# Kernel optimization log

Measured on AMD Instinct MI355X. Metric: run time of the kernel, lower is better.

Reference implementation:

```python
import jax, jax.numpy as jnp
import numpy as np

B, T, K = 512, 1024, 48


def setup_inputs() -> dict:
    key = jax.random.key(0)
    k1, k2, k3, k4, k5, k6 = jax.random.split(key, 6)
    return {
        "emission_scores": jax.random.normal(k1, (B, T, K), dtype=jnp.float32),
        "lengths": jax.random.randint(k2, (B,), 1, T + 1, dtype=jnp.int64),
        "tags": jax.random.randint(k3, (B, T), 0, K, dtype=jnp.int64),
        "prior": 0.1 * jax.random.normal(k4, (K,), dtype=jnp.float32),
        "transition": 0.1 * jax.random.normal(k5, (K, K), dtype=jnp.float32),
        "final_transition": 0.1 * jax.random.normal(k6, (K,), dtype=jnp.float32),
    }


def _partition_function(emission_scores, lengths, prior, transition, final_transition):
    batch, timesteps, num_tags = emission_scores.shape
    # alpha_0[b, i] = emis[b, 0, i] + prior[i]
    alpha0 = emission_scores[:, 0, :] + prior[None, :]

    def step(prev_alpha, emis_t):
        # alpha_t[b, i] = logsumexp_j(prev_alpha[b, j] + transition[i, j]) + emis_t[b, i]
        a = jax.nn.logsumexp(prev_alpha[:, None, :] + transition[None, :, :], axis=2)
        a = a + emis_t
        return a, a

    emis_rest = jnp.swapaxes(emission_scores, 0, 1)[1:]  # [T-1, B, K]
    _, alphas = jax.lax.scan(step, alpha0, emis_rest)
    alphas = jnp.concatenate([alpha0[None], alphas], axis=0)  # [T, B, K]
    alpha_final = alphas[lengths - 1, jnp.arange(batch)]  # [B, K] at last valid step
    alpha_final = alpha_final + final_transition[None, :]
    return jax.nn.logsumexp(alpha_final, axis=1)


def _score_path(emission_scores, lengths, tags, prior, transition, final_transition):
    batch, timesteps, num_tags = emission_scores.shape
    emis_tag = jnp.take_along_axis(emission_scores, tags[:, :, None], axis=2)[..., 0]  # [B, T]
    trans = transition[tags[:, 1:], tags[:, :-1]]  # [B, T-1]
    pr = prior[tags[:, 0]][:, None]  # [B, 1]
    scores = jnp.concatenate([pr, trans], axis=1) + emis_tag  # [B, T]
    valid = jnp.arange(timesteps)[None, :] < lengths[:, None]  # True for t < length
    scores = jnp.where(valid, scores, 0.0)
    final_tags = tags[jnp.arange(batch), lengths - 1]
    return jnp.sum(scores, axis=1) + final_transition[final_tags]


def reference(emission_scores, lengths, tags, prior, transition, final_transition):
    lengths = jnp.clip(lengths, 1, None)
    logZ = _partition_function(emission_scores, lengths, prior, transition, final_transition)
    path = _score_path(emission_scores, lengths, tags, prior, transition, final_transition)
    return jnp.mean(logZ - path)
```

## Files before the change

kernel.cpp:

```cpp
#include <hip/hip_runtime.h>


#define BB    512
#define TT    1024
#define KK    48
#define GG    16
#define NGRP  32
#define NSLOT 16
#define SLOTB (13 * GG * 16)
#define PHASE 8
#define BLKT  256

typedef __attribute__((ext_vector_type(4))) short bf16x4;
typedef __attribute__((ext_vector_type(4))) float f32x4;
typedef __attribute__((ext_vector_type(4))) int   i32x4;

__device__ __forceinline__ f32x4 mfma16(bf16x4 a, bf16x4 b, f32x4 c) {
#if __has_builtin(__builtin_amdgcn_mfma_f32_16x16x16bf16_1k)
    return __builtin_amdgcn_mfma_f32_16x16x16bf16_1k(a, b, c, 0, 0, 0);
#else
    f32x4 d;
    asm volatile("v_mfma_f32_16x16x16_bf16 %0, %1, %2, %3"
                 : "=v"(d) : "v"(a), "v"(b), "v"(c));
    return d;
#endif
}

#if __has_builtin(__builtin_amdgcn_cvt_pk_bf16_f32)
typedef __attribute__((ext_vector_type(2))) __bf16 bf16x2_v;
__device__ __forceinline__ unsigned pk2(float lo, float hi) {
    union { bf16x2_v v; unsigned u; } x;
    x.v = __builtin_amdgcn_cvt_pk_bf16_f32(lo, hi);
    return x.u;
}
#else
__device__ __forceinline__ unsigned pk2(float lo, float hi) {
    return __builtin_amdgcn_perm(__float_as_uint(hi) + 0x8000u,
                                 __float_as_uint(lo) + 0x8000u,
                                 0x07060302u);
}
#endif
__device__ __forceinline__ bf16x4 pack4(float a, float b, float c, float d) {
    union { unsigned u[2]; bf16x4 v; } x;
    x.u[0] = pk2(a, b);
    x.u[1] = pk2(c, d);
    return x.v;
}

#if __has_builtin(__builtin_amdgcn_permlane16_swap)
__device__ __forceinline__ float swap16_max(float x) {
    auto p = __builtin_amdgcn_permlane16_swap(__float_as_int(x),
                                              __float_as_int(x), false, false);
    return fmaxf(__int_as_float(p[0]), __int_as_float(p[1]));
}
__device__ __forceinline__ float swap16_sum(float x) {
    auto p = __builtin_amdgcn_permlane16_swap(__float_as_int(x),
                                              __float_as_int(x), false, false);
    return __int_as_float(p[0]) + __int_as_float(p[1]);
}
#else
__device__ __forceinline__ float swap16_max(float x) { return fmaxf(x, __shfl_xor(x, 16, 64)); }
__device__ __forceinline__ float swap16_sum(float x) { return x + __shfl_xor(x, 16, 64); }
#endif
#if __has_builtin(__builtin_amdgcn_permlane32_swap)
__device__ __forceinline__ float swap32_max(float x) {
    auto p = __builtin_amdgcn_permlane32_swap(__float_as_int(x),
                                              __float_as_int(x), false, false);
    return fmaxf(__int_as_float(p[0]), __int_as_float(p[1]));
}
__device__ __forceinline__ float swap32_sum(float x) {
    auto p = __builtin_amdgcn_permlane32_swap(__float_as_int(x),
                                              __float_as_int(x), false, false);
    return __int_as_float(p[0]) + __int_as_float(p[1]);
}
#else
__device__ __forceinline__ float swap32_max(float x) { return fmaxf(x, __shfl_xor(x, 32, 64)); }
__device__ __forceinline__ float swap32_sum(float x) { return x + __shfl_xor(x, 32, 64); }
#endif

__device__ __forceinline__ float wave_reduce_sum(float v) {
    #pragma unroll
    for (int off = 32; off > 0; off >>= 1)
        v += __shfl_xor(v, off, 64);
    return v;
}

__global__ __launch_bounds__(BLKT, 1) void crf_main_kernel(
    const float* __restrict__ emis,
    const int*   __restrict__ lengths,
    const int*   __restrict__ tags,
    const float* __restrict__ prior,
    const float* __restrict__ trans,
    const float* __restrict__ finalT,
    float*       __restrict__ ws)
{
    __shared__ __align__(16) unsigned char ring[NSLOT * SLOTB];
    __shared__ __align__(16) int prodCnt4[4];
    __shared__ int consCnt;

    const int tid  = threadIdx.x;
    const int wv   = tid >> 6;
    const int lane = tid & 63;

    if (blockIdx.x >= NGRP) {
        const int b = blockIdx.x - NGRP;
        int len = lengths[b];
        len = (len < 1) ? 1 : (len > TT ? TT : len);
        const float* eb = emis + (size_t)b * TT * KK;
        const int*   tg = tags + (size_t)b * TT;
        float ps = 0.0f;
        for (int t = tid; t < len; t += BLKT) {
            int cur = tg[t];
            float ev = eb[(size_t)t * KK + cur];
            float tr = (t == 0) ? prior[cur] : trans[cur * KK + tg[t - 1]];
            ps += ev + tr;
        }
        ps = wave_reduce_sum(ps);
        float* red = (float*)ring;
        if (lane == 0) red[wv] = ps;
        __syncthreads();
        if (tid == 0)
            ws[BB + b] = red[0] + red[1] + red[2] + red[3] + finalT[tg[len - 1]];
        return;
    }

    const int g = blockIdx.x;
    __builtin_amdgcn_s_setprio(1);

    if (tid == 0) {
        prodCnt4[0] = 0; prodCnt4[1] = 0; prodCnt4[2] = 0; prodCnt4[3] = 0;
        consCnt = 0;
    }
    __syncthreads();

    int myLen = lengths[g * GG + (lane & 15)];
    myLen = (myLen < 1) ? 1 : (myLen > TT ? TT : myLen);
    int gmax = myLen;
    #pragma unroll
    for (int off = 32; off > 0; off >>= 1) {
        int o = __shfl_xor(gmax, off, 64);
        gmax = (o > gmax) ? o : gmax;
    }
    const int nsteps = gmax - 1;
    const int nphase = (nsteps + PHASE - 1) / PHASE;

    if (wv >= 1) {
        const float* gp[3]; int lo[3];
        #pragma unroll
        for (int j = 0; j < 3; ++j) {
            int lidx = lane + 64 * j;
            int s    = lidx / 12;
            int kg   = lidx - s * 12;
            gp[j]    = emis + (size_t)(g * GG + s) * (TT * KK) + kg * 4;
            lo[j]    = (s * 13 + kg) * 16;
        }
        const int sA = wv - 1;
        float4 LA[9], LB[9];

#define PLOADX(Lb, KP)                                                     \
        {                                                                  \
            _Pragma("unroll")                                              \
            for (int h = 0; h < 3; ++h) {                                  \
                int s = sA + 3 * h;                                        \
                if (s < PHASE) {                                           \
                    int t  = 1 + (KP) * PHASE + s;                         \
                    int tc = (t > nsteps) ? nsteps : t;                    \
                    _Pragma("unroll")                                      \
                    for (int j = 0; j < 3; ++j)                            \
                        Lb[h * 3 + j] = *reinterpret_cast<const float4*>(  \
                            gp[j] + (size_t)tc * KK);                      \
                }                                                          \
            }                                                              \
        }

#define PSTORE(Lb, SB)                                                     \
        {                                                                  \
            _Pragma("unroll")                                              \
            for (int h = 0; h < 3; ++h) {                                  \
                int s = sA + 3 * h;                                        \
                if (s < PHASE) {                                           \
                    unsigned char* bp =                                    \
                        &ring[(((SB) + s) & (NSLOT - 1)) * SLOTB];         \
                    _Pragma("unroll")                                      \
                    for (int j = 0; j < 3; ++j) {                          \
                        float4 l = Lb[h * 3 + j];                          \
                        float4 e;                                          \
                        e.x = __expf(l.x); e.y = __expf(l.y);              \
                        e.z = __expf(l.z); e.w = __expf(l.w);              \
                        *reinterpret_cast<float4*>(bp + lo[j]) = e;        \
                    }                                                      \
                }                                                          \
            }                                                              \
        }

        PLOADX(LA, 0);
        PLOADX(LB, 1);
        volatile int* vc = &consCnt;
        for (int k0 = 0; k0 < nphase; k0 += 2) {
            while (*vc < k0 - 1) __builtin_amdgcn_s_sleep(1);
            asm volatile("" ::: "memory");
            PSTORE(LA, 1);
            asm volatile("s_waitcnt lgkmcnt(0)" ::: "memory");
            if (lane == 0) *(volatile int*)&prodCnt4[sA] = k0 + 1;
            asm volatile("" ::: "memory");
            PLOADX(LA, k0 + 2);
            if (k0 + 1 < nphase) {
                while (*vc < k0) __builtin_amdgcn_s_sleep(1);
                asm volatile("" ::: "memory");
                PSTORE(LB, 9);
                asm volatile("s_waitcnt lgkmcnt(0)" ::: "memory");
                if (lane == 0) *(volatile int*)&prodCnt4[sA] = k0 + 2;
                asm volatile("" ::: "memory");
                PLOADX(LB, k0 + 3);
            }
        }
#undef PLOADX
#undef PSTORE
        return;
    }

    const int col   = lane & 15;
    const int grp   = lane >> 4;
    const int rbase = grp * 4;
    const int seq   = g * GG + col;
    const int lenn1 = myLen - 1;

    bf16x4 A[3][3];
    #pragma unroll
    for (int mt = 0; mt < 3; ++mt) {
        #pragma unroll
        for (int kt = 0; kt < 3; ++kt) {
            float4 tv = *reinterpret_cast<const float4*>(
                trans + (size_t)(mt * 16 + col) * KK + kt * 16 + rbase);
            A[mt][kt] = pack4(__expf(tv.x), __expf(tv.y),
                              __expf(tv.z), __expf(tv.w));
        }
    }

    f32x4 EF[3];
    #pragma unroll
    for (int mt = 0; mt < 3; ++mt) {
        float4 fv = *reinterpret_cast<const float4*>(finalT + mt * 16 + rbase);
        EF[mt][0] = __expf(fv.x); EF[mt][1] = __expf(fv.y);
        EF[mt][2] = __expf(fv.z); EF[mt][3] = __expf(fv.w);
    }

    const float* ebase = emis + (size_t)seq * TT * KK + rbase;

    float c;
    float zcap = 0.0f;
    bf16x4 Bt0, Bt1, Bt2;
    {
        f32x4 a0[3];
        #pragma unroll
        for (int mt = 0; mt < 3; ++mt) {
            f32x4 ev = *reinterpret_cast<const f32x4*>(ebase + mt * 16);
            f32x4 pv = *reinterpret_cast<const f32x4*>(prior + mt * 16 + rbase);
            a0[mt] = ev + pv;
        }
        float mx = fmaxf(
            fmaxf(fmaxf(fmaxf(a0[0][0], a0[0][1]), fmaxf(a0[0][2], a0[0][3])),
                  fmaxf(fmaxf(a0[1][0], a0[1][1]), fmaxf(a0[1][2], a0[1][3]))),
            fmaxf(fmaxf(a0[2][0], a0[2][1]), fmaxf(a0[2][2], a0[2][3])));
        mx = swap16_max(mx);
        mx = swap32_max(mx);
        c = mx;
        #pragma unroll
        for (int mt = 0; mt < 3; ++mt) {
            #pragma unroll
            for (int e = 0; e < 4; ++e) a0[mt][e] = __expf(a0[mt][e] - c);
        }
        if (__ballot(lenn1 == 0)) {
            f32x4 Sv = a0[0] * EF[0] + a0[1] * EF[1] + a0[2] * EF[2];
            float S = (Sv[0] + Sv[1]) + (Sv[2] + Sv[3]);
            S = swap16_sum(S);
            S = swap32_sum(S);
            if (lenn1 == 0) zcap = c + __logf(S);
        }
        Bt0 = pack4(a0[0][0], a0[0][1], a0[0][2], a0[0][3]);
        Bt1 = pack4(a0[1][0], a0[1][1], a0[1][2], a0[1][3]);
        Bt2 = pack4(a0[2][0], a0[2][1], a0[2][2], a0[2][3]);
    }

    const int foff = col * 52 + grp * 4;
    const f32x4 zero4 = {0.f, 0.f, 0.f, 0.f};

#define XLOAD(dst, SLOT)                                                   \
        {                                                                  \
            const float* sp = reinterpret_cast<const float*>(              \
                ring + (SLOT) * SLOTB) + foff;                             \
            dst[0] = *reinterpret_cast<const f32x4*>(sp);                  \
            dst[1] = *reinterpret_cast<const f32x4*>(sp + 16);             \
            dst[2] = *reinterpret_cast<const f32x4*>(sp + 32);             \
        }

#define CPHASE(K_, SB)                                                       \
    {                                                                        \
        const int kc = (K_);                                                 \
        for (;;) {                            \
            i32x4 f = *(volatile i32x4*)prodCnt4;                            \
            if (f[0] >= kc + 1 && f[1] >= kc + 1 && f[2] >= kc + 1) break;   \
        }                                                                    \
        asm volatile("" ::: "memory");                                       \
        const int t0 = 1 + kc * PHASE;                                       \
        f32x4 Xq[PHASE + 2][3];                                              \
        XLOAD(Xq[0], ((SB) + 0) & (NSLOT - 1));                              \
        XLOAD(Xq[1], ((SB) + 1) & (NSLOT - 1));                              \
        _Pragma("unroll")                                                    \
        for (int s8 = 0; s8 < PHASE; ++s8) {                                 \
            if (s8 + 2 < PHASE)                        \
                XLOAD(Xq[s8 + 2], ((SB) + s8 + 2) & (NSLOT - 1));            \
            if (s8 == PHASE - 1) {                                           \
                  \
                asm volatile("s_waitcnt lgkmcnt(0)" ::: "memory");           \
                if (lane == 0) *(volatile int*)&consCnt = kc + 1;            \
                asm volatile("" ::: "memory");                               \
            }                                                                \
            const int t = t0 + s8;                \
            f32x4 D0 = mfma16(A[0][0], Bt0, zero4);                          \
            f32x4 D1 = mfma16(A[1][0], Bt0, zero4);                          \
            f32x4 D2 = mfma16(A[2][0], Bt0, zero4);                          \
            D0 = mfma16(A[0][1], Bt1, D0);                                   \
            D1 = mfma16(A[1][1], Bt1, D1);                                   \
            D2 = mfma16(A[2][1], Bt1, D2);                                   \
            D0 = mfma16(A[0][2], Bt2, D0);                                   \
            D1 = mfma16(A[1][2], Bt2, D1);                                   \
            D2 = mfma16(A[2][2], Bt2, D2);                                   \
            f32x4 Wa = D0 * Xq[s8][0];              \
            f32x4 Wb = D1 * Xq[s8][1];                                       \
            f32x4 Wc = D2 * Xq[s8][2];                                       \
            if (s8 == PHASE - 1) {                    \
                float mx = fmaxf(                                            \
                    fmaxf(fmaxf(fmaxf(Wa[0], Wa[1]), fmaxf(Wa[2], Wa[3])),   \
                          fmaxf(fmaxf(Wb[0], Wb[1]), fmaxf(Wb[2], Wb[3]))),  \
                    fmaxf(fmaxf(Wc[0], Wc[1]), fmaxf(Wc[2], Wc[3])));        \
                mx = swap16_max(mx);                                         \
                mx = swap32_max(mx);                                         \
                c += __logf(mx);                                             \
                float rm = __builtin_amdgcn_rcpf(mx);                        \
                Wa *= rm; Wb *= rm; Wc *= rm;                                \
            }                                                                \
            if (__ballot(t == lenn1)) {                    \
                f32x4 Sv = Wa * EF[0] + Wb * EF[1] + Wc * EF[2];             \
                float S = (Sv[0] + Sv[1]) + (Sv[2] + Sv[3]);                 \
                S = swap16_sum(S);                                           \
                S = swap32_sum(S);                                           \
                if (t == lenn1) zcap = c + __logf(S);                        \
            }                                                                \
            Bt0 = pack4(Wa[0], Wa[1], Wa[2], Wa[3]);                         \
            Bt1 = pack4(Wb[0], Wb[1], Wb[2], Wb[3]);                         \
            Bt2 = pack4(Wc[0], Wc[1], Wc[2], Wc[3]);                         \
        }                                                                    \
    }

    for (int k0 = 0; k0 < nphase; k0 += 2) {
        CPHASE(k0, 1);
        if (k0 + 1 < nphase) CPHASE(k0 + 1, 9);
    }
#undef CPHASE
#undef XLOAD

    if (lane < GG) ws[seq] = zcap;
}

__global__ __launch_bounds__(512) void reduce_mean_kernel(
    const float* __restrict__ ws, float* __restrict__ out)
{
    __shared__ float sm[8];
    int tid = threadIdx.x;
    float x = ws[tid] - ws[BB + tid];
    x = wave_reduce_sum(x);
    if ((tid & 63) == 0) sm[tid >> 6] = x;
    __syncthreads();
    if (tid < 8) {
        float y = sm[tid];
        y += __shfl_xor(y, 1, 64);
        y += __shfl_xor(y, 2, 64);
        y += __shfl_xor(y, 4, 64);
        if (tid == 0) out[0] = y * (1.0f / 512.0f);
    }
}

extern "C" void kernel_launch(void* const* d_in, const int* in_sizes, int n_in,
                              void* d_out, int out_size, void* d_ws, size_t ws_size,
                              hipStream_t stream) {
    const float* emis    = (const float*)d_in[0];
    const int*   lengths = (const int*)  d_in[1];
    const int*   tags    = (const int*)  d_in[2];
    const float* prior   = (const float*)d_in[3];
    const float* trans   = (const float*)d_in[4];
    const float* finalT  = (const float*)d_in[5];

    float* ws  = (float*)d_ws;
    float* out = (float*)d_out;

    crf_main_kernel<<<NGRP + BB, BLKT, 0, stream>>>(emis, lengths, tags, prior,
                                                    trans, finalT, ws);
    reduce_mean_kernel<<<1, 512, 0, stream>>>(ws, out);
}
```

Before: 303.8 us.

## Process two sequence groups per consumer wave with interleaved MFMA chains

Each consumer block now handles 32 sequences as two independent 16-column recurrences, interleaving their MFMA chains so one chain's latency is hidden behind the other. The number of group blocks is halved, the phase shrinks from 8 to 4 steps, and the ring shrinks to 8 slots. Producer waves compute exp before waiting, and the consumer uses inline-asm LDS reads with explicit waitcnt and templated capture dispatch. The trade-off is fewer concurrent recurrence blocks and more register pressure per wave, in exchange for better MFMA pipeline utilisation.

```diff
diff --git a/kernel.cpp b/kernel.cpp
--- a/kernel.cpp
+++ b/kernel.cpp
@@ -4,11 +4,11 @@
 #define BB    512
 #define TT    1024
 #define KK    48
-#define GG    16
-#define NGRP  32
-#define NSLOT 16
-#define SLOTB (13 * GG * 16)
-#define PHASE 8
+#define GG2   32
+#define NGRP2 16
+#define NSLOT 8
+#define SLOTB (415 * 16)
+#define PHASE 4
 #define BLKT  256
 
 typedef __attribute__((ext_vector_type(4))) short bf16x4;
@@ -47,7 +47,7 @@
     return x.v;
 }
 
-#if __has_builtin(__builtin_amdgcn_permlane16_swap)
+#if __has_builtin(__builtin_amdgcn_permlane16_swap) && __has_builtin(__builtin_amdgcn_permlane32_swap)
 __device__ __forceinline__ float swap16_max(float x) {
     auto p = __builtin_amdgcn_permlane16_swap(__float_as_int(x),
                                               __float_as_int(x), false, false);
@@ -58,11 +58,6 @@
                                               __float_as_int(x), false, false);
     return __int_as_float(p[0]) + __int_as_float(p[1]);
 }
-#else
-__device__ __forceinline__ float swap16_max(float x) { return fmaxf(x, __shfl_xor(x, 16, 64)); }
-__device__ __forceinline__ float swap16_sum(float x) { return x + __shfl_xor(x, 16, 64); }
-#endif
-#if __has_builtin(__builtin_amdgcn_permlane32_swap)
 __device__ __forceinline__ float swap32_max(float x) {
     auto p = __builtin_amdgcn_permlane32_swap(__float_as_int(x),
                                               __float_as_int(x), false, false);
@@ -74,6 +69,8 @@
     return __int_as_float(p[0]) + __int_as_float(p[1]);
 }
 #else
+__device__ __forceinline__ float swap16_max(float x) { return fmaxf(x, __shfl_xor(x, 16, 64)); }
+__device__ __forceinline__ float swap16_sum(float x) { return x + __shfl_xor(x, 16, 64); }
 __device__ __forceinline__ float swap32_max(float x) { return fmaxf(x, __shfl_xor(x, 32, 64)); }
 __device__ __forceinline__ float swap32_sum(float x) { return x + __shfl_xor(x, 32, 64); }
 #endif
@@ -83,6 +80,129 @@
     for (int off = 32; off > 0; off >>= 1)
         v += __shfl_xor(v, off, 64);
     return v;
+}
+
+#define WAITLGKM(N) asm volatile("s_waitcnt lgkmcnt(" #N ")" ::: "memory")
+#define SCHEDB()    __builtin_amdgcn_sched_barrier(0)
+
+template<int OFF>
+__device__ __forceinline__ void xread(unsigned base, f32x4& a, f32x4& b, f32x4& c3) {
+    asm volatile("ds_read_b128 %0, %3 offset:%c4\n\t"
+                 "ds_read_b128 %1, %3 offset:%c5\n\t"
+                 "ds_read_b128 %2, %3 offset:%c6"
+                 : "=&v"(a), "=&v"(b), "=&v"(c3)
+                 : "v"(base), "i"(OFF), "i"(OFF + 64), "i"(OFF + 128));
+}
+
+template<bool RESC, bool CAP0, bool CAP1>
+__device__ __forceinline__ void dual_step(
+    const bf16x4 (&A)[3][3], const f32x4 (&EF)[3],
+    bf16x4 (&Bt)[2][3], float (&c)[2], float (&zc)[2], const int (&ln)[2],
+    const f32x4 (&X0)[3], const f32x4 (&X1)[3], int t)
+{
+    const f32x4 z4 = {0.f, 0.f, 0.f, 0.f};
+    f32x4 d0 = mfma16(A[0][0], Bt[0][0], z4);
+    f32x4 d1 = mfma16(A[1][0], Bt[0][0], z4);
+    f32x4 d2 = mfma16(A[2][0], Bt[0][0], z4);
+    f32x4 e0 = mfma16(A[0][0], Bt[1][0], z4);
+    f32x4 e1 = mfma16(A[1][0], Bt[1][0], z4);
+    f32x4 e2 = mfma16(A[2][0], Bt[1][0], z4);
+    d0 = mfma16(A[0][1], Bt[0][1], d0);
+    d1 = mfma16(A[1][1], Bt[0][1], d1);
+    d2 = mfma16(A[2][1], Bt[0][1], d2);
+    e0 = mfma16(A[0][1], Bt[1][1], e0);
+    e1 = mfma16(A[1][1], Bt[1][1], e1);
+    e2 = mfma16(A[2][1], Bt[1][1], e2);
+    d0 = mfma16(A[0][2], Bt[0][2], d0);
+    d1 = mfma16(A[1][2], Bt[0][2], d1);
+    d2 = mfma16(A[2][2], Bt[0][2], d2);
+    e0 = mfma16(A[0][2], Bt[1][2], e0);
+    e1 = mfma16(A[1][2], Bt[1][2], e1);
+    e2 = mfma16(A[2][2], Bt[1][2], e2);
+
+    f32x4 Wa = d0 * X0[0], Wb = d1 * X0[1], Wc = d2 * X0[2];
+    f32x4 Va = e0 * X1[0], Vb = e1 * X1[1], Vc = e2 * X1[2];
+
+    if (RESC) {
+        float m0 = fmaxf(
+            fmaxf(fmaxf(fmaxf(Wa[0], Wa[1]), fmaxf(Wa[2], Wa[3])),
+                  fmaxf(fmaxf(Wb[0], Wb[1]), fmaxf(Wb[2], Wb[3]))),
+            fmaxf(fmaxf(Wc[0], Wc[1]), fmaxf(Wc[2], Wc[3])));
+        float m1 = fmaxf(
+            fmaxf(fmaxf(fmaxf(Va[0], Va[1]), fmaxf(Va[2], Va[3])),
+                  fmaxf(fmaxf(Vb[0], Vb[1]), fmaxf(Vb[2], Vb[3]))),
+            fmaxf(fmaxf(Vc[0], Vc[1]), fmaxf(Vc[2], Vc[3])));
+        m0 = swap16_max(m0); m1 = swap16_max(m1);
+        m0 = swap32_max(m0); m1 = swap32_max(m1);
+        c[0] += __logf(m0);
+        c[1] += __logf(m1);
+        float r0 = __builtin_amdgcn_rcpf(m0);
+        float r1 = __builtin_amdgcn_rcpf(m1);
+        Wa *= r0; Wb *= r0; Wc *= r0;
+        Va *= r1; Vb *= r1; Vc *= r1;
+    }
+    if (CAP0) {
+        if (__ballot(t == ln[0])) {
+            f32x4 Sv = Wa * EF[0] + Wb * EF[1] + Wc * EF[2];
+            float S = (Sv[0] + Sv[1]) + (Sv[2] + Sv[3]);
+            S = swap16_sum(S);
+            S = swap32_sum(S);
+            if (t == ln[0]) zc[0] = c[0] + __logf(S);
+        }
+    }
+    if (CAP1) {
+        if (__ballot(t == ln[1])) {
+            f32x4 Sv = Va * EF[0] + Vb * EF[1] + Vc * EF[2];
+            float S = (Sv[0] + Sv[1]) + (Sv[2] + Sv[3]);
+            S = swap16_sum(S);
+            S = swap32_sum(S);
+            if (t == ln[1]) zc[1] = c[1] + __logf(S);
+        }
+    }
+    Bt[0][0] = pack4(Wa[0], Wa[1], Wa[2], Wa[3]);
+    Bt[0][1] = pack4(Wb[0], Wb[1], Wb[2], Wb[3]);
+    Bt[0][2] = pack4(Wc[0], Wc[1], Wc[2], Wc[3]);
+    Bt[1][0] = pack4(Va[0], Va[1], Va[2], Va[3]);
+    Bt[1][1] = pack4(Vb[0], Vb[1], Vb[2], Vb[3]);
+    Bt[1][2] = pack4(Vc[0], Vc[1], Vc[2], Vc[3]);
+}
+
+template<int SB, bool RESC, bool CAP0, bool CAP1>
+__device__ __forceinline__ void cons_phase(
+    int kc, unsigned xb0, unsigned xb1, unsigned flagAddr, unsigned consAddr,
+    int lane, const bf16x4 (&A)[3][3], const f32x4 (&EF)[3],
+    bf16x4 (&Bt)[2][3], float (&c)[2], float (&zc)[2], const int (&ln)[2])
+{
+    for (;;) {
+        i32x4 f;
+        asm volatile("ds_read_b128 %0, %1\n\ts_waitcnt lgkmcnt(0)"
+                     : "=&v"(f) : "v"(flagAddr) : "memory");
+        SCHEDB();
+        if (f[0] >= kc + 1 && f[1] >= kc + 1 && f[2] >= kc + 1) break;
+    }
+    const int t0 = 1 + kc * PHASE;
+    constexpr int O0 = ((SB + 0) & 7) * SLOTB;
+    constexpr int O1 = ((SB + 1) & 7) * SLOTB;
+    constexpr int O2 = ((SB + 2) & 7) * SLOTB;
+    constexpr int O3 = ((SB + 3) & 7) * SLOTB;
+    f32x4 X[PHASE][2][3];
+    xread<O0>(xb0, X[0][0][0], X[0][0][1], X[0][0][2]);
+    xread<O0>(xb1, X[0][1][0], X[0][1][1], X[0][1][2]);
+    xread<O1>(xb0, X[1][0][0], X[1][0][1], X[1][0][2]);
+    xread<O1>(xb1, X[1][1][0], X[1][1][1], X[1][1][2]);
+    xread<O2>(xb0, X[2][0][0], X[2][0][1], X[2][0][2]);
+    xread<O2>(xb1, X[2][1][0], X[2][1][1], X[2][1][2]);
+    WAITLGKM(12); SCHEDB();
+    dual_step<false, CAP0, CAP1>(A, EF, Bt, c, zc, ln, X[0][0], X[0][1], t0 + 0);
+    xread<O3>(xb0, X[3][0][0], X[3][0][1], X[3][0][2]);
+    xread<O3>(xb1, X[3][1][0], X[3][1][1], X[3][1][2]);
+    WAITLGKM(12); SCHEDB();
+    dual_step<false, CAP0, CAP1>(A, EF, Bt, c, zc, ln, X[1][0], X[1][1], t0 + 1);
+    WAITLGKM(0); SCHEDB();
+    if (lane == 0)
+        asm volatile("ds_write_b32 %0, %1" :: "v"(consAddr), "v"(kc + 1) : "memory");
+    dual_step<false, CAP0, CAP1>(A, EF, Bt, c, zc, ln, X[2][0], X[2][1], t0 + 2);
+    dual_step<RESC, CAP0, CAP1>(A, EF, Bt, c, zc, ln, X[3][0], X[3][1], t0 + 3);
 }
 
 __global__ __launch_bounds__(BLKT, 1) void crf_main_kernel(
@@ -102,8 +222,8 @@
     const int wv   = tid >> 6;
     const int lane = tid & 63;
 
-    if (blockIdx.x >= NGRP) {
-        const int b = blockIdx.x - NGRP;
+    if (blockIdx.x >= NGRP2) {
+        const int b = blockIdx.x - NGRP2;
         int len = lengths[b];
         len = (len < 1) ? 1 : (len > TT ? TT : len);
         const float* eb = emis + (size_t)b * TT * KK;
@@ -125,7 +245,6 @@
     }
 
     const int g = blockIdx.x;
-    __builtin_amdgcn_s_setprio(1);
 
     if (tid == 0) {
         prodCnt4[0] = 0; prodCnt4[1] = 0; prodCnt4[2] = 0; prodCnt4[3] = 0;
@@ -133,9 +252,9 @@
     }
     __syncthreads();
 
-    int myLen = lengths[g * GG + (lane & 15)];
-    myLen = (myLen < 1) ? 1 : (myLen > TT ? TT : myLen);
-    int gmax = myLen;
+    int myLenL = lengths[g * GG2 + (lane & 31)];
+    myLenL = (myLenL < 1) ? 1 : (myLenL > TT ? TT : myLenL);
+    int gmax = myLenL;
     #pragma unroll
     for (int off = 32; off > 0; off >>= 1) {
         int o = __shfl_xor(gmax, off, 64);
@@ -145,85 +264,104 @@
     const int nphase = (nsteps + PHASE - 1) / PHASE;
 
     if (wv >= 1) {
-        const float* gp[3]; int lo[3];
+        const int p = wv - 1;
+        const float* gp[6]; int lo[6];
         #pragma unroll
-        for (int j = 0; j < 3; ++j) {
-            int lidx = lane + 64 * j;
-            int s    = lidx / 12;
-            int kg   = lidx - s * 12;
-            gp[j]    = emis + (size_t)(g * GG + s) * (TT * KK) + kg * 4;
-            lo[j]    = (s * 13 + kg) * 16;
-        }
-        const int sA = wv - 1;
-        float4 LA[9], LB[9];
-
-#define PLOADX(Lb, KP)                                                     \
-        {                                                                  \
+        for (int q = 0; q < 6; ++q) {
+            int gidx = lane + 64 * q;
+            int s    = gidx / 12;
+            int kg   = gidx - s * 12;
+            gp[q]    = emis + (size_t)(g * GG2 + s) * (TT * KK) + kg * 4;
+            lo[q]    = (s * 13 + kg) * 16;
+        }
+        const float* g3p[2]; int lo3[2];
+        #pragma unroll
+        for (int q = 0; q < 2; ++q) {
+            int gidx = 128 * p + lane + 64 * q;
+            int s    = gidx / 12;
+            int kg   = gidx - s * 12;
+            g3p[q]   = emis + (size_t)(g * GG2 + s) * (TT * KK) + kg * 4;
+            lo3[q]   = (s * 13 + kg) * 16;
+        }
+        float4 PB0[8], PB1[8];
+
+#define PLOAD(buf, KP)                                                     \
+        do {                                                               \
+            int tp = 1 + 4 * (KP) + p;  tp = (tp > nsteps) ? nsteps : tp;  \
+            int t3 = 1 + 4 * (KP) + 3;  t3 = (t3 > nsteps) ? nsteps : t3;  \
             _Pragma("unroll")                                              \
-            for (int h = 0; h < 3; ++h) {                                  \
-                int s = sA + 3 * h;                                        \
-                if (s < PHASE) {                                           \
-                    int t  = 1 + (KP) * PHASE + s;                         \
-                    int tc = (t > nsteps) ? nsteps : t;                    \
-                    _Pragma("unroll")                                      \
-                    for (int j = 0; j < 3; ++j)                            \
-                        Lb[h * 3 + j] = *reinterpret_cast<const float4*>(  \
-                            gp[j] + (size_t)tc * KK);                      \
-                }                                                          \
+            for (int q = 0; q < 6; ++q)                                    \
+                buf[q] = *reinterpret_cast<const float4*>(                 \
+                    gp[q] + (size_t)tp * KK);                              \
+            buf[6] = *reinterpret_cast<const float4*>(g3p[0] + (size_t)t3 * KK); \
+            buf[7] = *reinterpret_cast<const float4*>(g3p[1] + (size_t)t3 * KK); \
+        } while (0)
+
+#define EXPIP(buf)                                                         \
+        do {                                                               \
+            _Pragma("unroll")                                              \
+            for (int q = 0; q < 8; ++q) {                                  \
+                float4 l = buf[q];                                         \
+                l.x = __expf(l.x); l.y = __expf(l.y);                      \
+                l.z = __expf(l.z); l.w = __expf(l.w);                      \
+                buf[q] = l;                                                \
             }                                                              \
-        }
-
-#define PSTORE(Lb, SB)                                                     \
-        {                                                                  \
+        } while (0)
+
+#define PSTORE(buf, SP, S3)                                                \
+        do {                                                               \
+            unsigned char* bp = &ring[(SP) * SLOTB];                       \
             _Pragma("unroll")                                              \
-            for (int h = 0; h < 3; ++h) {                                  \
-                int s = sA + 3 * h;                                        \
-                if (s < PHASE) {                                           \
-                    unsigned char* bp =                                    \
-                        &ring[(((SB) + s) & (NSLOT - 1)) * SLOTB];         \
-                    _Pragma("unroll")                                      \
-                    for (int j = 0; j < 3; ++j) {                          \
-                        float4 l = Lb[h * 3 + j];                          \
-                        float4 e;                                          \
-                        e.x = __expf(l.x); e.y = __expf(l.y);              \
-                        e.z = __expf(l.z); e.w = __expf(l.w);              \
-                        *reinterpret_cast<float4*>(bp + lo[j]) = e;        \
-                    }                                                      \
-                }                                                          \
-            }                                                              \
-        }
-
-        PLOADX(LA, 0);
-        PLOADX(LB, 1);
+            for (int q = 0; q < 6; ++q)                                    \
+                *reinterpret_cast<float4*>(bp + lo[q]) = buf[q];           \
+            unsigned char* b3 = &ring[(S3) * SLOTB];                       \
+            *reinterpret_cast<float4*>(b3 + lo3[0]) = buf[6];              \
+            *reinterpret_cast<float4*>(b3 + lo3[1]) = buf[7];              \
+        } while (0)
+
+        PLOAD(PB0, 0);
+        PLOAD(PB1, 1);
+        EXPIP(PB0);
         volatile int* vc = &consCnt;
         for (int k0 = 0; k0 < nphase; k0 += 2) {
             while (*vc < k0 - 1) __builtin_amdgcn_s_sleep(1);
             asm volatile("" ::: "memory");
-            PSTORE(LA, 1);
+            PSTORE(PB0, 1 + p, 4);
             asm volatile("s_waitcnt lgkmcnt(0)" ::: "memory");
-            if (lane == 0) *(volatile int*)&prodCnt4[sA] = k0 + 1;
+            if (lane == 0) *(volatile int*)&prodCnt4[p] = k0 + 1;
             asm volatile("" ::: "memory");
-            PLOADX(LA, k0 + 2);
+            PLOAD(PB0, k0 + 2);
+            EXPIP(PB1);
             if (k0 + 1 < nphase) {
                 while (*vc < k0) __builtin_amdgcn_s_sleep(1);
                 asm volatile("" ::: "memory");
-                PSTORE(LB, 9);
+                PSTORE(PB1, 5 + p, 0);
                 asm volatile("s_waitcnt lgkmcnt(0)" ::: "memory");
-                if (lane == 0) *(volatile int*)&prodCnt4[sA] = k0 + 2;
+                if (lane == 0) *(volatile int*)&prodCnt4[p] = k0 + 2;
                 asm volatile("" ::: "memory");
-                PLOADX(LB, k0 + 3);
+                PLOAD(PB1, k0 + 3);
+                EXPIP(PB0);
             }
         }
-#undef PLOADX
+#undef PLOAD
+#undef EXPIP
 #undef PSTORE
         return;
     }
 
+    __builtin_amdgcn_s_setprio(1);
     const int col   = lane & 15;
     const int grp   = lane >> 4;
     const int rbase = grp * 4;
-    const int seq   = g * GG + col;
-    const int lenn1 = myLen - 1;
+    const int seq0  = g * GG2 + col;
+    const int seq1  = g * GG2 + 16 + col;
+
+    int ln[2];
+    {
+        int l0 = lengths[seq0]; l0 = (l0 < 1) ? 1 : (l0 > TT ? TT : l0);
+        int l1 = lengths[seq1]; l1 = (l1 < 1) ? 1 : (l1 > TT ? TT : l1);
+        ln[0] = l0 - 1; ln[1] = l1 - 1;
+    }
 
     bf16x4 A[3][3];
     #pragma unroll
@@ -236,7 +374,6 @@
                               __expf(tv.z), __expf(tv.w));
         }
     }
-
     f32x4 EF[3];
     #pragma unroll
     for (int mt = 0; mt < 3; ++mt) {
@@ -245,16 +382,16 @@
         EF[mt][2] = __expf(fv.z); EF[mt][3] = __expf(fv.w);
     }
 
-    const float* ebase = emis + (size_t)seq * TT * KK + rbase;
-
-    float c;
-    float zcap = 0.0f;
-    bf16x4 Bt0, Bt1, Bt2;
-    {
+    bf16x4 Bt[2][3];
+    float  c[2], zc[2];
+    zc[0] = 0.0f; zc[1] = 0.0f;
+    #pragma unroll
+    for (int q = 0; q < 2; ++q) {
+        const float* eb = emis + (size_t)(q ? seq1 : seq0) * TT * KK + rbase;
         f32x4 a0[3];
         #pragma unroll
         for (int mt = 0; mt < 3; ++mt) {
-            f32x4 ev = *reinterpret_cast<const f32x4*>(ebase + mt * 16);
+            f32x4 ev = *reinterpret_cast<const f32x4*>(eb + mt * 16);
             f32x4 pv = *reinterpret_cast<const f32x4*>(prior + mt * 16 + rbase);
             a0[mt] = ev + pv;
         }
@@ -264,103 +401,58 @@
             fmaxf(fmaxf(a0[2][0], a0[2][1]), fmaxf(a0[2][2], a0[2][3])));
         mx = swap16_max(mx);
         mx = swap32_max(mx);
-        c = mx;
+        c[q] = mx;
         #pragma unroll
         for (int mt = 0; mt < 3; ++mt) {
             #pragma unroll
-            for (int e = 0; e < 4; ++e) a0[mt][e] = __expf(a0[mt][e] - c);
-        }
-        if (__ballot(lenn1 == 0)) {
+            for (int e = 0; e < 4; ++e) a0[mt][e] = __expf(a0[mt][e] - mx);
+        }
+        if (__ballot(ln[q] == 0)) {
             f32x4 Sv = a0[0] * EF[0] + a0[1] * EF[1] + a0[2] * EF[2];
             float S = (Sv[0] + Sv[1]) + (Sv[2] + Sv[3]);
             S = swap16_sum(S);
             S = swap32_sum(S);
-            if (lenn1 == 0) zcap = c + __logf(S);
-        }
-        Bt0 = pack4(a0[0][0], a0[0][1], a0[0][2], a0[0][3]);
-        Bt1 = pack4(a0[1][0], a0[1][1], a0[1][2], a0[1][3]);
-        Bt2 = pack4(a0[2][0], a0[2][1], a0[2][2], a0[2][3]);
-    }
-
-    const int foff = col * 52 + grp * 4;
-    const f32x4 zero4 = {0.f, 0.f, 0.f, 0.f};
-
-#define XLOAD(dst, SLOT)                                                   \
-        {                                                                  \
-            const float* sp = reinterpret_cast<const float*>(              \
-                ring + (SLOT) * SLOTB) + foff;                             \
-            dst[0] = *reinterpret_cast<const f32x4*>(sp);                  \
-            dst[1] = *reinterpret_cast<const f32x4*>(sp + 16);             \
-            dst[2] = *reinterpret_cast<const f32x4*>(sp + 32);             \
-        }
-
-#define CPHASE(K_, SB)                                                       \
+            if (ln[q] == 0) zc[q] = mx + __logf(S);
+        }
+        Bt[q][0] = pack4(a0[0][0], a0[0][1], a0[0][2], a0[0][3]);
+        Bt[q][1] = pack4(a0[1][0], a0[1][1], a0[1][2], a0[1][3]);
+        Bt[q][2] = pack4(a0[2][0], a0[2][1], a0[2][2], a0[2][3]);
+    }
+
+    const unsigned xb0 = (unsigned)(size_t)&ring[0]
+                       + (unsigned)((col * 13 + grp) * 16);
+    const unsigned xb1 = xb0 + 3328u;
+    const unsigned flagAddr = (unsigned)(size_t)&prodCnt4[0];
+    const unsigned consAddr = (unsigned)(size_t)&consCnt;
+
+#define DISPATCH(KC, SBv, RESCv)                                             \
     {                                                                        \
-        const int kc = (K_);                                                 \
-        for (;;) {                            \
-            i32x4 f = *(volatile i32x4*)prodCnt4;                            \
-            if (f[0] >= kc + 1 && f[1] >= kc + 1 && f[2] >= kc + 1) break;   \
+        const int tt0 = 1 + (KC) * PHASE;                                    \
+        const bool ca = __ballot(ln[0] >= tt0 && ln[0] < tt0 + PHASE) != 0;  \
+        const bool cb = __ballot(ln[1] >= tt0 && ln[1] < tt0 + PHASE) != 0;  \
+        if (ca) {                                                            \
+            if (cb) cons_phase<SBv, RESCv, true,  true >(KC, xb0, xb1,       \
+                flagAddr, consAddr, lane, A, EF, Bt, c, zc, ln);             \
+            else    cons_phase<SBv, RESCv, true,  false>(KC, xb0, xb1,       \
+                flagAddr, consAddr, lane, A, EF, Bt, c, zc, ln);             \
+        } else {                                                             \
+            if (cb) cons_phase<SBv, RESCv, false, true >(KC, xb0, xb1,       \
+                flagAddr, consAddr, lane, A, EF, Bt, c, zc, ln);             \
+            else    cons_phase<SBv, RESCv, false, false>(KC, xb0, xb1,       \
+                flagAddr, consAddr, lane, A, EF, Bt, c, zc, ln);             \
         }                                                                    \
-        asm volatile("" ::: "memory");                                       \
-        const int t0 = 1 + kc * PHASE;                                       \
-        f32x4 Xq[PHASE + 2][3];                                              \
-        XLOAD(Xq[0], ((SB) + 0) & (NSLOT - 1));                              \
-        XLOAD(Xq[1], ((SB) + 1) & (NSLOT - 1));                              \
-        _Pragma("unroll")                                                    \
-        for (int s8 = 0; s8 < PHASE; ++s8) {                                 \
-            if (s8 + 2 < PHASE)                        \
-                XLOAD(Xq[s8 + 2], ((SB) + s8 + 2) & (NSLOT - 1));            \
-            if (s8 == PHASE - 1) {                                           \
-                  \
-                asm volatile("s_waitcnt lgkmcnt(0)" ::: "memory");           \
-                if (lane == 0) *(volatile int*)&consCnt = kc + 1;            \
-                asm volatile("" ::: "memory");                               \
-            }                                                                \
-            const int t = t0 + s8;                \
-            f32x4 D0 = mfma16(A[0][0], Bt0, zero4);                          \
-            f32x4 D1 = mfma16(A[1][0], Bt0, zero4);                          \
-            f32x4 D2 = mfma16(A[2][0], Bt0, zero4);                          \
-            D0 = mfma16(A[0][1], Bt1, D0);                                   \
-            D1 = mfma16(A[1][1], Bt1, D1);                                   \
-            D2 = mfma16(A[2][1], Bt1, D2);                                   \
-            D0 = mfma16(A[0][2], Bt2, D0);                                   \
-            D1 = mfma16(A[1][2], Bt2, D1);                                   \
-            D2 = mfma16(A[2][2], Bt2, D2);                                   \
-            f32x4 Wa = D0 * Xq[s8][0];              \
-            f32x4 Wb = D1 * Xq[s8][1];                                       \
-            f32x4 Wc = D2 * Xq[s8][2];                                       \
-            if (s8 == PHASE - 1) {                    \
-                float mx = fmaxf(                                            \
-                    fmaxf(fmaxf(fmaxf(Wa[0], Wa[1]), fmaxf(Wa[2], Wa[3])),   \
-                          fmaxf(fmaxf(Wb[0], Wb[1]), fmaxf(Wb[2], Wb[3]))),  \
-                    fmaxf(fmaxf(Wc[0], Wc[1]), fmaxf(Wc[2], Wc[3])));        \
-                mx = swap16_max(mx);                                         \
-                mx = swap32_max(mx);                                         \
-                c += __logf(mx);                                             \
-                float rm = __builtin_amdgcn_rcpf(mx);                        \
-                Wa *= rm; Wb *= rm; Wc *= rm;                                \
-            }                                                                \
-            if (__ballot(t == lenn1)) {                    \
-                f32x4 Sv = Wa * EF[0] + Wb * EF[1] + Wc * EF[2];             \
-                float S = (Sv[0] + Sv[1]) + (Sv[2] + Sv[3]);                 \
-                S = swap16_sum(S);                                           \
-                S = swap32_sum(S);                                           \
-                if (t == lenn1) zcap = c + __logf(S);                        \
-            }                                                                \
-            Bt0 = pack4(Wa[0], Wa[1], Wa[2], Wa[3]);                         \
-            Bt1 = pack4(Wb[0], Wb[1], Wb[2], Wb[3]);                         \
-            Bt2 = pack4(Wc[0], Wc[1], Wc[2], Wc[3]);                         \
-        }                                                                    \
     }
 
     for (int k0 = 0; k0 < nphase; k0 += 2) {
-        CPHASE(k0, 1);
-        if (k0 + 1 < nphase) CPHASE(k0 + 1, 9);
-    }
-#undef CPHASE
-#undef XLOAD
-
-    if (lane < GG) ws[seq] = zcap;
+        DISPATCH(k0, 1, false);
+        if (k0 + 1 < nphase) DISPATCH(k0 + 1, 5, true);
+    }
+#undef DISPATCH
+
+    if (lane < 16) {
+        ws[seq0] = zc[0];
+        ws[seq1] = zc[1];
+    }
 }
 
 __global__ __launch_bounds__(512) void reduce_mean_kernel(
@@ -394,7 +486,7 @@
     float* ws  = (float*)d_ws;
     float* out = (float*)d_out;
 
-    crf_main_kernel<<<NGRP + BB, BLKT, 0, stream>>>(emis, lengths, tags, prior,
-                                                    trans, finalT, ws);
+    crf_main_kernel<<<NGRP2 + BB, BLKT, 0, stream>>>(emis, lengths, tags, prior,
+                                                     trans, finalT, ws);
     reduce_mean_kernel<<<1, 512, 0, stream>>>(ws, out);
 }
```

New measurement: 459.2 us. 1.51x slower.

## Replace producer-wave LDS ring with single-wave register double-buffered emission prefetch

Applied to the files above, without the earlier changes.

Drops the warp-specialized design, where three producer waves loaded emissions, exponentiated them and wrote them to an LDS ring guarded by spin-wait counters. Now the one consumer wave loads its own emission rows straight from global memory into two register buffers, each covering a 4-step phase, and computes the exponentials inline before the MFMA recurrence. The final-step capture check is hoisted to one ballot per phase via template specialization, and rescaling now happens once every two phases. This removes the LDS traffic and the inter-wave spin synchronization, but puts the exp work and the global-load latency on the serial wave, with a shorter prefetch distance.

```diff
diff --git a/kernel.cpp b/kernel.cpp
--- a/kernel.cpp
+++ b/kernel.cpp
@@ -4,16 +4,12 @@
 #define BB    512
 #define TT    1024
 #define KK    48
-#define GG    16
 #define NGRP  32
-#define NSLOT 16
-#define SLOTB (13 * GG * 16)
-#define PHASE 8
+#define PH    4
 #define BLKT  256
 
 typedef __attribute__((ext_vector_type(4))) short bf16x4;
 typedef __attribute__((ext_vector_type(4))) float f32x4;
-typedef __attribute__((ext_vector_type(4))) int   i32x4;
 
 __device__ __forceinline__ f32x4 mfma16(bf16x4 a, bf16x4 b, f32x4 c) {
 #if __has_builtin(__builtin_amdgcn_mfma_f32_16x16x16bf16_1k)
@@ -47,7 +43,7 @@
     return x.v;
 }
 
-#if __has_builtin(__builtin_amdgcn_permlane16_swap)
+#if __has_builtin(__builtin_amdgcn_permlane16_swap) && __has_builtin(__builtin_amdgcn_permlane32_swap)
 __device__ __forceinline__ float swap16_max(float x) {
     auto p = __builtin_amdgcn_permlane16_swap(__float_as_int(x),
                                               __float_as_int(x), false, false);
@@ -58,11 +54,6 @@
                                               __float_as_int(x), false, false);
     return __int_as_float(p[0]) + __int_as_float(p[1]);
 }
-#else
-__device__ __forceinline__ float swap16_max(float x) { return fmaxf(x, __shfl_xor(x, 16, 64)); }
-__device__ __forceinline__ float swap16_sum(float x) { return x + __shfl_xor(x, 16, 64); }
-#endif
-#if __has_builtin(__builtin_amdgcn_permlane32_swap)
 __device__ __forceinline__ float swap32_max(float x) {
     auto p = __builtin_amdgcn_permlane32_swap(__float_as_int(x),
                                               __float_as_int(x), false, false);
@@ -74,6 +65,8 @@
     return __int_as_float(p[0]) + __int_as_float(p[1]);
 }
 #else
+__device__ __forceinline__ float swap16_max(float x) { return fmaxf(x, __shfl_xor(x, 16, 64)); }
+__device__ __forceinline__ float swap16_sum(float x) { return x + __shfl_xor(x, 16, 64); }
 __device__ __forceinline__ float swap32_max(float x) { return fmaxf(x, __shfl_xor(x, 32, 64)); }
 __device__ __forceinline__ float swap32_sum(float x) { return x + __shfl_xor(x, 32, 64); }
 #endif
@@ -83,6 +76,62 @@
     for (int off = 32; off > 0; off >>= 1)
         v += __shfl_xor(v, off, 64);
     return v;
+}
+
+__device__ __forceinline__ f32x4 exp4(f32x4 x) {
+    f32x4 r;
+    r[0] = __expf(x[0]); r[1] = __expf(x[1]);
+    r[2] = __expf(x[2]); r[3] = __expf(x[3]);
+    return r;
+}
+
+template<bool RESC, bool CAP>
+__device__ __forceinline__ void run_phase(
+    int t0, const f32x4 (&X)[PH][3],
+    const bf16x4 (&A)[3][3], const f32x4 (&EF)[3],
+    bf16x4& Bt0, bf16x4& Bt1, bf16x4& Bt2,
+    float& c, float& zc, int ln)
+{
+    const f32x4 z4 = {0.f, 0.f, 0.f, 0.f};
+    #pragma unroll
+    for (int S = 0; S < PH; ++S) {
+        f32x4 E0 = exp4(X[S][0]);
+        f32x4 E1 = exp4(X[S][1]);
+        f32x4 E2 = exp4(X[S][2]);
+        f32x4 d0 = mfma16(A[0][0], Bt0, z4);
+        f32x4 d1 = mfma16(A[1][0], Bt0, z4);
+        f32x4 d2 = mfma16(A[2][0], Bt0, z4);
+        d0 = mfma16(A[0][1], Bt1, d0);
+        d1 = mfma16(A[1][1], Bt1, d1);
+        d2 = mfma16(A[2][1], Bt1, d2);
+        d0 = mfma16(A[0][2], Bt2, d0);
+        d1 = mfma16(A[1][2], Bt2, d1);
+        d2 = mfma16(A[2][2], Bt2, d2);
+        f32x4 Wa = d0 * E0, Wb = d1 * E1, Wc = d2 * E2;
+        if (RESC && S == PH - 1) {
+            float mx = fmaxf(
+                fmaxf(fmaxf(fmaxf(Wa[0], Wa[1]), fmaxf(Wa[2], Wa[3])),
+                      fmaxf(fmaxf(Wb[0], Wb[1]), fmaxf(Wb[2], Wb[3]))),
+                fmaxf(fmaxf(Wc[0], Wc[1]), fmaxf(Wc[2], Wc[3])));
+            mx = swap16_max(mx);
+            mx = swap32_max(mx);
+            c += __logf(mx);
+            float rm = __builtin_amdgcn_rcpf(mx);
+            Wa *= rm; Wb *= rm; Wc *= rm;
+        }
+        if (CAP) {
+            if (__ballot(t0 + S == ln)) {
+                f32x4 Sv = Wa * EF[0] + Wb * EF[1] + Wc * EF[2];
+                float Ssum = (Sv[0] + Sv[1]) + (Sv[2] + Sv[3]);
+                Ssum = swap16_sum(Ssum);
+                Ssum = swap32_sum(Ssum);
+                if (t0 + S == ln) zc = c + __logf(Ssum);
+            }
+        }
+        Bt0 = pack4(Wa[0], Wa[1], Wa[2], Wa[3]);
+        Bt1 = pack4(Wb[0], Wb[1], Wb[2], Wb[3]);
+        Bt2 = pack4(Wc[0], Wc[1], Wc[2], Wc[3]);
+    }
 }
 
 __global__ __launch_bounds__(BLKT, 1) void crf_main_kernel(
@@ -94,9 +143,7 @@
     const float* __restrict__ finalT,
     float*       __restrict__ ws)
 {
-    __shared__ __align__(16) unsigned char ring[NSLOT * SLOTB];
-    __shared__ __align__(16) int prodCnt4[4];
-    __shared__ int consCnt;
+    __shared__ float red[4];
 
     const int tid  = threadIdx.x;
     const int wv   = tid >> 6;
@@ -116,7 +163,6 @@
             ps += ev + tr;
         }
         ps = wave_reduce_sum(ps);
-        float* red = (float*)ring;
         if (lane == 0) red[wv] = ps;
         __syncthreads();
         if (tid == 0)
@@ -124,106 +170,26 @@
         return;
     }
 
-    const int g = blockIdx.x;
+    if (wv != 0) return;
     __builtin_amdgcn_s_setprio(1);
 
-    if (tid == 0) {
-        prodCnt4[0] = 0; prodCnt4[1] = 0; prodCnt4[2] = 0; prodCnt4[3] = 0;
-        consCnt = 0;
-    }
-    __syncthreads();
-
-    int myLen = lengths[g * GG + (lane & 15)];
-    myLen = (myLen < 1) ? 1 : (myLen > TT ? TT : myLen);
-    int gmax = myLen;
-    #pragma unroll
-    for (int off = 32; off > 0; off >>= 1) {
-        int o = __shfl_xor(gmax, off, 64);
-        gmax = (o > gmax) ? o : gmax;
-    }
-    const int nsteps = gmax - 1;
-    const int nphase = (nsteps + PHASE - 1) / PHASE;
-
-    if (wv >= 1) {
-        const float* gp[3]; int lo[3];
-        #pragma unroll
-        for (int j = 0; j < 3; ++j) {
-            int lidx = lane + 64 * j;
-            int s    = lidx / 12;
-            int kg   = lidx - s * 12;
-            gp[j]    = emis + (size_t)(g * GG + s) * (TT * KK) + kg * 4;
-            lo[j]    = (s * 13 + kg) * 16;
-        }
-        const int sA = wv - 1;
-        float4 LA[9], LB[9];
-
-#define PLOADX(Lb, KP)                                                     \
-        {                                                                  \
-            _Pragma("unroll")                                              \
-            for (int h = 0; h < 3; ++h) {                                  \
-                int s = sA + 3 * h;                                        \
-                if (s < PHASE) {                                           \
-                    int t  = 1 + (KP) * PHASE + s;                         \
-                    int tc = (t > nsteps) ? nsteps : t;                    \
-                    _Pragma("unroll")                                      \
-                    for (int j = 0; j < 3; ++j)                            \
-                        Lb[h * 3 + j] = *reinterpret_cast<const float4*>(  \
-                            gp[j] + (size_t)tc * KK);                      \
-                }                                                          \
-            }                                                              \
-        }
-
-#define PSTORE(Lb, SB)                                                     \
-        {                                                                  \
-            _Pragma("unroll")                                              \
-            for (int h = 0; h < 3; ++h) {                                  \
-                int s = sA + 3 * h;                                        \
-                if (s < PHASE) {                                           \
-                    unsigned char* bp =                                    \
-                        &ring[(((SB) + s) & (NSLOT - 1)) * SLOTB];         \
-                    _Pragma("unroll")                                      \
-                    for (int j = 0; j < 3; ++j) {                          \
-                        float4 l = Lb[h * 3 + j];                          \
-                        float4 e;                                          \
-                        e.x = __expf(l.x); e.y = __expf(l.y);              \
-                        e.z = __expf(l.z); e.w = __expf(l.w);              \
-                        *reinterpret_cast<float4*>(bp + lo[j]) = e;        \
-                    }                                                      \
-                }                                                          \
-            }                                                              \
-        }
-
-        PLOADX(LA, 0);
-        PLOADX(LB, 1);
-        volatile int* vc = &consCnt;
-        for (int k0 = 0; k0 < nphase; k0 += 2) {
-            while (*vc < k0 - 1) __builtin_amdgcn_s_sleep(1);
-            asm volatile("" ::: "memory");
-            PSTORE(LA, 1);
-            asm volatile("s_waitcnt lgkmcnt(0)" ::: "memory");
-            if (lane == 0) *(volatile int*)&prodCnt4[sA] = k0 + 1;
-            asm volatile("" ::: "memory");
-            PLOADX(LA, k0 + 2);
-            if (k0 + 1 < nphase) {
-                while (*vc < k0) __builtin_amdgcn_s_sleep(1);
-                asm volatile("" ::: "memory");
-                PSTORE(LB, 9);
-                asm volatile("s_waitcnt lgkmcnt(0)" ::: "memory");
-                if (lane == 0) *(volatile int*)&prodCnt4[sA] = k0 + 2;
-                asm volatile("" ::: "memory");
-                PLOADX(LB, k0 + 3);
-            }
-        }
-#undef PLOADX
-#undef PSTORE
-        return;
-    }
-
+    const int g     = blockIdx.x;
     const int col   = lane & 15;
     const int grp   = lane >> 4;
     const int rbase = grp * 4;
-    const int seq   = g * GG + col;
-    const int lenn1 = myLen - 1;
+    const int seq   = g * 16 + col;
+
+    int myLen = lengths[seq];
+    myLen = (myLen < 1) ? 1 : (myLen > TT ? TT : myLen);
+    const int ln = myLen - 1;
+    int gm = myLen;
+    #pragma unroll
+    for (int off = 1; off < 16; off <<= 1) {
+        int o = __shfl_xor(gm, off, 64);
+        gm = (o > gm) ? o : gm;
+    }
+    const int nsteps = __builtin_amdgcn_readfirstlane(gm) - 1;
+    const int nphase = (nsteps + PH - 1) / PH;
 
     bf16x4 A[3][3];
     #pragma unroll
@@ -236,7 +202,6 @@
                               __expf(tv.z), __expf(tv.w));
         }
     }
-
     f32x4 EF[3];
     #pragma unroll
     for (int mt = 0; mt < 3; ++mt) {
@@ -245,16 +210,15 @@
         EF[mt][2] = __expf(fv.z); EF[mt][3] = __expf(fv.w);
     }
 
-    const float* ebase = emis + (size_t)seq * TT * KK + rbase;
-
-    float c;
-    float zcap = 0.0f;
+    const float* eb_lane = emis + (size_t)seq * TT * KK + rbase;
+
     bf16x4 Bt0, Bt1, Bt2;
+    float  c, zc = 0.0f;
     {
         f32x4 a0[3];
         #pragma unroll
         for (int mt = 0; mt < 3; ++mt) {
-            f32x4 ev = *reinterpret_cast<const f32x4*>(ebase + mt * 16);
+            f32x4 ev = *reinterpret_cast<const f32x4*>(eb_lane + mt * 16);
             f32x4 pv = *reinterpret_cast<const f32x4*>(prior + mt * 16 + rbase);
             a0[mt] = ev + pv;
         }
@@ -268,99 +232,55 @@
         #pragma unroll
         for (int mt = 0; mt < 3; ++mt) {
             #pragma unroll
-            for (int e = 0; e < 4; ++e) a0[mt][e] = __expf(a0[mt][e] - c);
-        }
-        if (__ballot(lenn1 == 0)) {
+            for (int e = 0; e < 4; ++e) a0[mt][e] = __expf(a0[mt][e] - mx);
+        }
+        if (__ballot(ln == 0)) {
             f32x4 Sv = a0[0] * EF[0] + a0[1] * EF[1] + a0[2] * EF[2];
-            float S = (Sv[0] + Sv[1]) + (Sv[2] + Sv[3]);
-            S = swap16_sum(S);
-            S = swap32_sum(S);
-            if (lenn1 == 0) zcap = c + __logf(S);
+            float Ssum = (Sv[0] + Sv[1]) + (Sv[2] + Sv[3]);
+            Ssum = swap16_sum(Ssum);
+            Ssum = swap32_sum(Ssum);
+            if (ln == 0) zc = mx + __logf(Ssum);
         }
         Bt0 = pack4(a0[0][0], a0[0][1], a0[0][2], a0[0][3]);
         Bt1 = pack4(a0[1][0], a0[1][1], a0[1][2], a0[1][3]);
         Bt2 = pack4(a0[2][0], a0[2][1], a0[2][2], a0[2][3]);
     }
 
-    const int foff = col * 52 + grp * 4;
-    const f32x4 zero4 = {0.f, 0.f, 0.f, 0.f};
-
-#define XLOAD(dst, SLOT)                                                   \
-        {                                                                  \
-            const float* sp = reinterpret_cast<const float*>(              \
-                ring + (SLOT) * SLOTB) + foff;                             \
-            dst[0] = *reinterpret_cast<const f32x4*>(sp);                  \
-            dst[1] = *reinterpret_cast<const f32x4*>(sp + 16);             \
-            dst[2] = *reinterpret_cast<const f32x4*>(sp + 32);             \
-        }
-
-#define CPHASE(K_, SB)                                                       \
-    {                                                                        \
-        const int kc = (K_);                                                 \
-        for (;;) {                            \
-            i32x4 f = *(volatile i32x4*)prodCnt4;                            \
-            if (f[0] >= kc + 1 && f[1] >= kc + 1 && f[2] >= kc + 1) break;   \
-        }                                                                    \
-        asm volatile("" ::: "memory");                                       \
-        const int t0 = 1 + kc * PHASE;                                       \
-        f32x4 Xq[PHASE + 2][3];                                              \
-        XLOAD(Xq[0], ((SB) + 0) & (NSLOT - 1));                              \
-        XLOAD(Xq[1], ((SB) + 1) & (NSLOT - 1));                              \
-        _Pragma("unroll")                                                    \
-        for (int s8 = 0; s8 < PHASE; ++s8) {                                 \
-            if (s8 + 2 < PHASE)                        \
-                XLOAD(Xq[s8 + 2], ((SB) + s8 + 2) & (NSLOT - 1));            \
-            if (s8 == PHASE - 1) {                                           \
-                  \
-                asm volatile("s_waitcnt lgkmcnt(0)" ::: "memory");           \
-                if (lane == 0) *(volatile int*)&consCnt = kc + 1;            \
-                asm volatile("" ::: "memory");                               \
-            }                                                                \
-            const int t = t0 + s8;                \
-            f32x4 D0 = mfma16(A[0][0], Bt0, zero4);                          \
-            f32x4 D1 = mfma16(A[1][0], Bt0, zero4);                          \
-            f32x4 D2 = mfma16(A[2][0], Bt0, zero4);                          \
-            D0 = mfma16(A[0][1], Bt1, D0);                                   \
-            D1 = mfma16(A[1][1], Bt1, D1);                                   \
-            D2 = mfma16(A[2][1], Bt1, D2);                                   \
-            D0 = mfma16(A[0][2], Bt2, D0);                                   \
-            D1 = mfma16(A[1][2], Bt2, D1);                                   \
-            D2 = mfma16(A[2][2], Bt2, D2);                                   \
-            f32x4 Wa = D0 * Xq[s8][0];              \
-            f32x4 Wb = D1 * Xq[s8][1];                                       \
-            f32x4 Wc = D2 * Xq[s8][2];                                       \
-            if (s8 == PHASE - 1) {                    \
-                float mx = fmaxf(                                            \
-                    fmaxf(fmaxf(fmaxf(Wa[0], Wa[1]), fmaxf(Wa[2], Wa[3])),   \
-                          fmaxf(fmaxf(Wb[0], Wb[1]), fmaxf(Wb[2], Wb[3]))),  \
-                    fmaxf(fmaxf(Wc[0], Wc[1]), fmaxf(Wc[2], Wc[3])));        \
-                mx = swap16_max(mx);                                         \
-                mx = swap32_max(mx);                                         \
-                c += __logf(mx);                                             \
-                float rm = __builtin_amdgcn_rcpf(mx);                        \
-                Wa *= rm; Wb *= rm; Wc *= rm;                                \
-            }                                                                \
-            if (__ballot(t == lenn1)) {                    \
-                f32x4 Sv = Wa * EF[0] + Wb * EF[1] + Wc * EF[2];             \
-                float S = (Sv[0] + Sv[1]) + (Sv[2] + Sv[3]);                 \
-                S = swap16_sum(S);                                           \
-                S = swap32_sum(S);                                           \
-                if (t == lenn1) zcap = c + __logf(S);                        \
-            }                                                                \
-            Bt0 = pack4(Wa[0], Wa[1], Wa[2], Wa[3]);                         \
-            Bt1 = pack4(Wb[0], Wb[1], Wb[2], Wb[3]);                         \
-            Bt2 = pack4(Wc[0], Wc[1], Wc[2], Wc[3]);                         \
-        }                                                                    \
-    }
-
-    for (int k0 = 0; k0 < nphase; k0 += 2) {
-        CPHASE(k0, 1);
-        if (k0 + 1 < nphase) CPHASE(k0 + 1, 9);
-    }
-#undef CPHASE
-#undef XLOAD
-
-    if (lane < GG) ws[seq] = zcap;
+    f32x4 XA[PH][3], XB[PH][3];
+
+#define LDPH(Xb, KP)                                                       \
+    do {                                                                   \
+        _Pragma("unroll")                                                  \
+        for (int S = 0; S < PH; ++S) {                                     \
+            int tc = 1 + PH * (KP) + S;                                    \
+            tc = (tc > nsteps) ? nsteps : tc;                              \
+            const float* pp = eb_lane + (size_t)tc * KK;                   \
+            Xb[S][0] = *reinterpret_cast<const f32x4*>(pp);                \
+            Xb[S][1] = *reinterpret_cast<const f32x4*>(pp + 16);           \
+            Xb[S][2] = *reinterpret_cast<const f32x4*>(pp + 32);           \
+        }                                                                  \
+    } while (0)
+
+    LDPH(XA, 0);
+    for (int k = 0; k < nphase; k += 2) {
+        LDPH(XB, k + 1);
+        {
+            const int t0 = 1 + k * PH;
+            const bool cap = __ballot(ln >= t0 && ln < t0 + PH) != 0;
+            if (cap) run_phase<false, true >(t0, XA, A, EF, Bt0, Bt1, Bt2, c, zc, ln);
+            else     run_phase<false, false>(t0, XA, A, EF, Bt0, Bt1, Bt2, c, zc, ln);
+        }
+        if (k + 1 < nphase) {
+            LDPH(XA, k + 2);
+            const int t0 = 1 + (k + 1) * PH;
+            const bool cap = __ballot(ln >= t0 && ln < t0 + PH) != 0;
+            if (cap) run_phase<true, true >(t0, XB, A, EF, Bt0, Bt1, Bt2, c, zc, ln);
+            else     run_phase<true, false>(t0, XB, A, EF, Bt0, Bt1, Bt2, c, zc, ln);
+        }
+    }
+#undef LDPH
+
+    if (lane < 16) ws[seq] = zc;
 }
 
 __global__ __launch_bounds__(512) void reduce_mean_kernel(
```

Measured after the change: 333.0 us. 1.1x slower.
